# Performance work log

Measured on AMD Instinct MI355X. Metric: run time of the kernel, lower is better.

## Reference

```python
import jax, jax.numpy as jnp
import numpy as np

NPOINT = 1024   # npoint
K = 20          # num_samples[0]


def _fps(pts, npoint):
    """Iterative furthest point sampling. pts: [N,3] -> indices [npoint] (starts at idx 0)."""
    N = pts.shape[0]

    def step(carry, _):
        min_d, last = carry
        d = jnp.sum((pts - pts[last]) ** 2, axis=-1)          # [N] dist to last selected
        min_d = jnp.minimum(min_d, d)                          # running min-dist to selected set
        nxt = jnp.argmax(min_d).astype(jnp.int32)
        return (min_d, nxt), nxt

    init = (jnp.full((N,), 1e10, pts.dtype), jnp.int32(0))
    _, rest = jax.lax.scan(step, init, None, length=npoint - 1)
    return jnp.concatenate([jnp.zeros((1,), jnp.int32), rest])


def _pdist2(q, p):
    """Squared pairwise distances. q:[M,3], p:[N,3] -> [M,N], clamped to >=0 (matches pdist2squared)."""
    d = jnp.sum(q * q, -1)[:, None] + jnp.sum(p * p, -1)[None, :] - 2.0 * (q @ p.T)
    return jnp.maximum(d, 0.0)


def _knn(q, p, k):
    """k nearest neighbors of each q among p, dropping the closest (self), ascending order."""
    d = _pdist2(q, p)                       # [M,N]
    _, idx = jax.lax.top_k(-d, k + 1)       # ascending distance order
    return idx[:, 1:]                       # drop self, [M,k]


def setup_inputs() -> dict:
    key = jax.random.key(0)
    points = jax.random.normal(key, (4, 16384, 3), dtype=jnp.float32)
    return {"points": points}


def reference(points):
    B, N, _ = points.shape
    # --- FPS node sampling (Sample module) ---
    xyz_ind = jax.vmap(lambda p: _fps(p, NPOINT))(points)                  # [B, N1]
    xyz_query = jnp.take_along_axis(points, xyz_ind[:, :, None], axis=1)  # [B, N1, 3]

    # --- Gmid: neighbors of the N1 query points among all N points ---
    nbr_mid = jax.vmap(lambda q, p: _knn(q, p, K))(xyz_query, points)      # [B, N1, K]
    src_mid = jnp.take_along_axis(points, nbr_mid.reshape(B, -1, 1), axis=1).reshape(B, NPOINT, K, 3)
    d_mid = xyz_query[:, :, None, :] - src_mid                             # edata['d'] = pos[dst]-pos[src]

    # --- Gout: neighbors among the downsampled N1 points themselves ---
    nbr_out = jax.vmap(lambda q: _knn(q, q, K))(xyz_query)                 # [B, N1, K]
    src_out = jnp.take_along_axis(xyz_query, nbr_out.reshape(B, -1, 1), axis=1).reshape(B, NPOINT, K, 3)
    d_out = xyz_query[:, :, None, :] - src_out

    return xyz_ind, xyz_query, nbr_mid, d_mid, nbr_out, d_out
```

## Files before the change

### kernel.cpp

```cpp
#include <hip/hip_runtime.h>
#include <stdint.h>

#define BATCH   4
#define NPTS    16384
#define NPOINT  1024
#define KNN     20
#define KSEL    21

typedef unsigned long long u64;

#define FPS_SUBS 16
#define FPS_TPB  256
#define FPS_GT   (FPS_SUBS * FPS_TPB)
#define FPS_PPT  (NPTS / FPS_GT)

#define REPEAT4(M) M(0) M(1) M(2) M(3)

#define FPS_DECL(i) float px##i, py##i, pz##i, md##i;

#define FPS_INIT(i) { \
    int idx = (i) * FPS_GT + g; \
    px##i = P[idx * 3 + 0]; \
    py##i = P[idx * 3 + 1]; \
    pz##i = P[idx * 3 + 2]; \
    md##i = 1e10f; }

#define FPS_STEP(i) { \
    float dx = __fsub_rn(px##i, qx); \
    float dy = __fsub_rn(py##i, qy); \
    float dz = __fsub_rn(pz##i, qz); \
    float d  = __fadd_rn(__fadd_rn(__fmul_rn(dx, dx), __fmul_rn(dy, dy)), \
                         __fmul_rn(dz, dz)); \
    float m = fminf(md##i, d); \
    md##i = m; \
    bool g2 = (m > best); \
    best = g2 ? m : best; \
    bi   = g2 ? (i) : bi; }

__global__ __launch_bounds__(FPS_TPB)
void fps_kernel(const float* __restrict__ pts, float* __restrict__ out,
                int* __restrict__ ws_ind, float* __restrict__ ws_query,
                u64* __restrict__ slots) {
  const int blk = blockIdx.x;
  const int b   = blk >> 4;
  const int sub = blk & 15;
  const int t   = threadIdx.x;
  const int g   = sub * FPS_TPB + t;
  const float* P = pts + (size_t)b * NPTS * 3;
  float* out_ind = out;
  float* out_q   = out + BATCH * NPOINT;

  REPEAT4(FPS_DECL)
  REPEAT4(FPS_INIT)

  __shared__ float s_val[FPS_TPB / 64];
  __shared__ int   s_idx[FPS_TPB / 64];
  __shared__ int   s_widx;

  if (sub == 0 && t == 0) {
    out_ind[b * NPOINT] = 0.0f;
    ws_ind[b * NPOINT]  = 0;
    float ax = P[0], ay = P[1], az = P[2];
    size_t o0 = (size_t)(b * NPOINT) * 3;
    out_q[o0 + 0] = ax; out_q[o0 + 1] = ay; out_q[o0 + 2] = az;
    ws_query[o0 + 0] = ax; ws_query[o0 + 1] = ay; ws_query[o0 + 2] = az;
  }
  float qx = P[0], qy = P[1], qz = P[2];

  for (int it = 1; it < NPOINT; ++it) {
    float best = -1.0f;
    int bi = 0;
    REPEAT4(FPS_STEP)
    int bidx = bi * FPS_GT + g;

#pragma unroll
    for (int off = 32; off >= 1; off >>= 1) {
      float ov = __shfl_down(best, off);
      int   oi = __shfl_down(bidx, off);
      if (ov > best || (ov == best && oi < bidx)) { best = ov; bidx = oi; }
    }
    if ((t & 63) == 0) { s_val[t >> 6] = best; s_idx[t >> 6] = bidx; }
    __syncthreads();

    if (t < 64) {
      float bv = s_val[0];
      int   bx = s_idx[0];
#pragma unroll
      for (int w = 1; w < FPS_TPB / 64; ++w) {
        float v = s_val[w];
        int   x = s_idx[w];
        if (v > bv || (v == bv && x < bx)) { bv = v; bx = x; }
      }
      u64* row = slots + (size_t)it * (BATCH * FPS_SUBS) + b * FPS_SUBS;
      if (t == 0) {
        u64 pv = ((u64)__float_as_uint(bv) << 32) |
                 (unsigned)(bx | (it << 20));
        __hip_atomic_store(&row[sub], pv, __ATOMIC_RELAXED,
                           __HIP_MEMORY_SCOPE_AGENT);
      }
      int j = t & 15;
      u64 v;
      do {
        v = __hip_atomic_load(&row[j], __ATOMIC_RELAXED,
                              __HIP_MEMORY_SCOPE_AGENT);
      } while ((v >> 63) != 0 ||
               (((unsigned)(v >> 20)) & 0x3FFu) != (unsigned)it);
      float fv = __uint_as_float((unsigned)(v >> 32));
      int   fi = (int)((unsigned)v & 0xFFFFFu);
#pragma unroll
      for (int off = 8; off >= 1; off >>= 1) {
        float ofv = __shfl_down(fv, off);
        int   ofi = __shfl_down(fi, off);
        if (ofv > fv || (ofv == fv && ofi < fi)) { fv = ofv; fi = ofi; }
      }
      if (t == 0) s_widx = fi;
    }
    __syncthreads();
    const int widx = s_widx;

    qx = P[widx * 3 + 0];
    qy = P[widx * 3 + 1];
    qz = P[widx * 3 + 2];

    if (sub == 0 && t == 0) {
      out_ind[b * NPOINT + it] = (float)widx;
      ws_ind[b * NPOINT + it]  = widx;
      size_t o = (size_t)(b * NPOINT + it) * 3;
      out_q[o + 0] = qx; out_q[o + 1] = qy; out_q[o + 2] = qz;
      ws_query[o + 0] = qx; ws_query[o + 1] = qy; ws_query[o + 2] = qz;
    }
  }
}

#define KNN_WAVES 4

__global__ __launch_bounds__(256)
void knn_kernel(const float* __restrict__ cand_base,
                const float* __restrict__ query_base,
                int ncand,
                float* __restrict__ out_nbr,
                float* __restrict__ out_d) {
#pragma clang fp contract(off)
  const int wid_in_blk = threadIdx.x >> 6;
  const int w    = blockIdx.x * KNN_WAVES + wid_in_blk;
  const int lane = threadIdx.x & 63;
  const int b    = w / NPOINT;
  const int qi   = w % NPOINT;

  const float* C = cand_base + (size_t)b * ncand * 3;
  const float* Q = query_base + ((size_t)b * NPOINT + qi) * 3;
  const float qx = Q[0], qy = Q[1], qz = Q[2];
  const float qq = (qx * qx + qy * qy) + qz * qz;

  unsigned long long best[KSEL];
#pragma unroll
  for (int j = 0; j < KSEL; ++j) best[j] = 0xFFFFFFFFFFFFFFFFull;

  for (int j = lane; j < ncand; j += 64) {
    float px = C[j * 3 + 0], py = C[j * 3 + 1], pz = C[j * 3 + 2];
    float pp  = (px * px + py * py) + pz * pz;
    float dot = __builtin_fmaf(qz, pz, __builtin_fmaf(qy, py, qx * px));
    float d = (qq + pp) - 2.0f * dot;
    d = fmaxf(d, 0.0f);
    unsigned long long key =
        ((unsigned long long)__float_as_uint(d) << 32) | (unsigned int)j;
    if (key < best[KSEL - 1]) {
      unsigned long long c = key;
#pragma unroll
      for (int s = 0; s < KSEL; ++s) {
        unsigned long long o = best[s];
        bool l = c < o;
        unsigned long long nb = l ? c : o;
        c = l ? o : c;
        best[s] = nb;
      }
    }
  }

  __shared__ unsigned long long s_list[KNN_WAVES][64 * KSEL];
  unsigned long long* L = s_list[wid_in_blk];
#pragma unroll
  for (int j = 0; j < KSEL; ++j) L[lane * KSEL + j] = best[j];
  __syncthreads();

  int hp = 0;
  int myK = -1, myIdx = 0;
  for (int r = 0; r < KSEL; ++r) {
    unsigned long long v = L[lane * KSEL + hp];
    int src = lane;
#pragma unroll
    for (int off = 32; off >= 1; off >>= 1) {
      unsigned long long ov = __shfl_down(v, off);
      int os = __shfl_down(src, off);
      if (ov < v) { v = ov; src = os; }
    }
    v   = __shfl(v, 0);
    src = __shfl(src, 0);
    if (lane == src) hp++;
    if (r >= 1 && lane == r - 1) {
      myIdx = (int)(unsigned int)(v & 0xFFFFFFFFull);
      myK = r - 1;
    }
  }

  if (myK >= 0) {
    size_t o = (size_t)(b * NPOINT + qi) * KNN + myK;
    out_nbr[o] = (float)myIdx;
    float sx = C[myIdx * 3 + 0], sy = C[myIdx * 3 + 1], sz = C[myIdx * 3 + 2];
    out_d[o * 3 + 0] = qx - sx;
    out_d[o * 3 + 1] = qy - sy;
    out_d[o * 3 + 2] = qz - sz;
  }
}

extern "C" void kernel_launch(void* const* d_in, const int* in_sizes, int n_in,
                              void* d_out, int out_size, void* d_ws,
                              size_t ws_size, hipStream_t stream) {
  (void)in_sizes; (void)n_in; (void)out_size; (void)ws_size;
  const float* pts = (const float*)d_in[0];
  float* out = (float*)d_out;

  int*   ws_ind   = (int*)d_ws;
  float* ws_query = (float*)((char*)d_ws + (size_t)BATCH * NPOINT * sizeof(int));
  u64*   slots    = (u64*)((char*)d_ws + 64 * 1024);

  float* out_nbr_mid = out + (size_t)BATCH * NPOINT * 4;
  float* out_d_mid   = out_nbr_mid + (size_t)BATCH * NPOINT * KNN;
  float* out_nbr_out = out_d_mid + (size_t)BATCH * NPOINT * KNN * 3;
  float* out_d_out   = out_nbr_out + (size_t)BATCH * NPOINT * KNN;

  hipLaunchKernelGGL(fps_kernel, dim3(BATCH * FPS_SUBS), dim3(FPS_TPB), 0,
                     stream, pts, out, ws_ind, ws_query, slots);

  hipLaunchKernelGGL(knn_kernel, dim3(BATCH * NPOINT / KNN_WAVES), dim3(256),
                     0, stream, pts, ws_query, NPTS, out_nbr_mid, out_d_mid);

  hipLaunchKernelGGL(knn_kernel, dim3(BATCH * NPOINT / KNN_WAVES), dim3(256),
                     0, stream, ws_query, ws_query, NPOINT, out_nbr_out,
                     out_d_out);
}
```

Measured before the change: 2.786 ms.

## Fuse FPS and mid-KNN into one kernel, overlapping KNN with FPS progress

Merges the FPS kernel and the first KNN kernel into one launch. Extra blocks spin on the per-iteration FPS slot records to learn each selected index, then run their KNN query over the full point set while FPS is still iterating. The KNN merge step now keeps candidate lists in registers and walks the list head instead of staging them in shared memory. This hides most of the mid-KNN time behind the serial FPS loop. The risks are that spinning blocks compete with FPS blocks for compute units, and that the scheme relies on all FPS blocks being resident at once to avoid deadlock.

```diff
diff --git a/kernel.cpp b/kernel.cpp
--- a/kernel.cpp
+++ b/kernel.cpp
@@ -11,8 +11,10 @@
 
 #define FPS_SUBS 16
 #define FPS_TPB  256
+#define FPS_BLOCKS (BATCH * FPS_SUBS)
 #define FPS_GT   (FPS_SUBS * FPS_TPB)
 #define FPS_PPT  (NPTS / FPS_GT)
+#define KNN_BLOCKS (BATCH * NPOINT / 4)
 
 #define REPEAT4(M) M(0) M(1) M(2) M(3)
 
@@ -38,73 +40,122 @@
     bi   = g2 ? (i) : bi; }
 
 __global__ __launch_bounds__(FPS_TPB)
-void fps_kernel(const float* __restrict__ pts, float* __restrict__ out,
-                int* __restrict__ ws_ind, float* __restrict__ ws_query,
-                u64* __restrict__ slots) {
-  const int blk = blockIdx.x;
-  const int b   = blk >> 4;
-  const int sub = blk & 15;
-  const int t   = threadIdx.x;
-  const int g   = sub * FPS_TPB + t;
-  const float* P = pts + (size_t)b * NPTS * 3;
-  float* out_ind = out;
-  float* out_q   = out + BATCH * NPOINT;
-
-  REPEAT4(FPS_DECL)
-  REPEAT4(FPS_INIT)
-
+void fused_kernel(const float* __restrict__ pts, float* __restrict__ out,
+                  int* __restrict__ ws_ind, float* __restrict__ ws_query,
+                  u64* __restrict__ slots,
+                  float* __restrict__ out_nbr_mid,
+                  float* __restrict__ out_d_mid) {
   __shared__ float s_val[FPS_TPB / 64];
   __shared__ int   s_idx[FPS_TPB / 64];
   __shared__ int   s_widx;
 
-  if (sub == 0 && t == 0) {
-    out_ind[b * NPOINT] = 0.0f;
-    ws_ind[b * NPOINT]  = 0;
-    float ax = P[0], ay = P[1], az = P[2];
-    size_t o0 = (size_t)(b * NPOINT) * 3;
-    out_q[o0 + 0] = ax; out_q[o0 + 1] = ay; out_q[o0 + 2] = az;
-    ws_query[o0 + 0] = ax; ws_query[o0 + 1] = ay; ws_query[o0 + 2] = az;
-  }
-  float qx = P[0], qy = P[1], qz = P[2];
-
-  for (int it = 1; it < NPOINT; ++it) {
-    float best = -1.0f;
-    int bi = 0;
-    REPEAT4(FPS_STEP)
-    int bidx = bi * FPS_GT + g;
-
-#pragma unroll
-    for (int off = 32; off >= 1; off >>= 1) {
-      float ov = __shfl_down(best, off);
-      int   oi = __shfl_down(bidx, off);
-      if (ov > best || (ov == best && oi < bidx)) { best = ov; bidx = oi; }
-    }
-    if ((t & 63) == 0) { s_val[t >> 6] = best; s_idx[t >> 6] = bidx; }
-    __syncthreads();
-
-    if (t < 64) {
-      float bv = s_val[0];
-      int   bx = s_idx[0];
-#pragma unroll
-      for (int w = 1; w < FPS_TPB / 64; ++w) {
-        float v = s_val[w];
-        int   x = s_idx[w];
-        if (v > bv || (v == bv && x < bx)) { bv = v; bx = x; }
-      }
-      u64* row = slots + (size_t)it * (BATCH * FPS_SUBS) + b * FPS_SUBS;
-      if (t == 0) {
-        u64 pv = ((u64)__float_as_uint(bv) << 32) |
-                 (unsigned)(bx | (it << 20));
-        __hip_atomic_store(&row[sub], pv, __ATOMIC_RELAXED,
-                           __HIP_MEMORY_SCOPE_AGENT);
-      }
-      int j = t & 15;
+  if (blockIdx.x < FPS_BLOCKS) {
+    const int blk = blockIdx.x;
+    const int b   = blk >> 4;
+    const int sub = blk & 15;
+    const int t   = threadIdx.x;
+    const int g   = sub * FPS_TPB + t;
+    const float* P = pts + (size_t)b * NPTS * 3;
+    float* out_ind = out;
+    float* out_q   = out + BATCH * NPOINT;
+
+    REPEAT4(FPS_DECL)
+    REPEAT4(FPS_INIT)
+
+    if (sub == 0 && t == 0) {
+      out_ind[b * NPOINT] = 0.0f;
+      ws_ind[b * NPOINT]  = 0;
+      float ax = P[0], ay = P[1], az = P[2];
+      size_t o0 = (size_t)(b * NPOINT) * 3;
+      out_q[o0 + 0] = ax; out_q[o0 + 1] = ay; out_q[o0 + 2] = az;
+      ws_query[o0 + 0] = ax; ws_query[o0 + 1] = ay; ws_query[o0 + 2] = az;
+    }
+    float qx = P[0], qy = P[1], qz = P[2];
+
+    for (int it = 1; it < NPOINT; ++it) {
+      float best = -1.0f;
+      int bi = 0;
+      REPEAT4(FPS_STEP)
+      int bidx = bi * FPS_GT + g;
+
+#pragma unroll
+      for (int off = 32; off >= 1; off >>= 1) {
+        float ov = __shfl_down(best, off);
+        int   oi = __shfl_down(bidx, off);
+        if (ov > best || (ov == best && oi < bidx)) { best = ov; bidx = oi; }
+      }
+      if ((t & 63) == 0) { s_val[t >> 6] = best; s_idx[t >> 6] = bidx; }
+      __syncthreads();
+
+      if (t < 64) {
+        float bv = s_val[0];
+        int   bx = s_idx[0];
+#pragma unroll
+        for (int w = 1; w < FPS_TPB / 64; ++w) {
+          float v = s_val[w];
+          int   x = s_idx[w];
+          if (v > bv || (v == bv && x < bx)) { bv = v; bx = x; }
+        }
+        u64* row = slots + (size_t)it * (BATCH * FPS_SUBS) + b * FPS_SUBS;
+        if (t == 0) {
+          u64 pv = ((u64)__float_as_uint(bv) << 32) |
+                   (unsigned)(bx | (it << 20));
+          __hip_atomic_store(&row[sub], pv, __ATOMIC_RELAXED,
+                             __HIP_MEMORY_SCOPE_AGENT);
+        }
+        int j = t & 15;
+        u64 v;
+        do {
+          v = __hip_atomic_load(&row[j], __ATOMIC_RELAXED,
+                                __HIP_MEMORY_SCOPE_AGENT);
+        } while ((v >> 63) != 0 ||
+                 (((unsigned)(v >> 20)) & 0x3FFu) != (unsigned)it);
+        float fv = __uint_as_float((unsigned)(v >> 32));
+        int   fi = (int)((unsigned)v & 0xFFFFFu);
+#pragma unroll
+        for (int off = 8; off >= 1; off >>= 1) {
+          float ofv = __shfl_down(fv, off);
+          int   ofi = __shfl_down(fi, off);
+          if (ofv > fv || (ofv == fv && ofi < fi)) { fv = ofv; fi = ofi; }
+        }
+        if (t == 0) s_widx = fi;
+      }
+      __syncthreads();
+      const int widx = s_widx;
+
+      qx = P[widx * 3 + 0];
+      qy = P[widx * 3 + 1];
+      qz = P[widx * 3 + 2];
+
+      if (sub == 0 && t == 0) {
+        out_ind[b * NPOINT + it] = (float)widx;
+        ws_ind[b * NPOINT + it]  = widx;
+        size_t o = (size_t)(b * NPOINT + it) * 3;
+        out_q[o + 0] = qx; out_q[o + 1] = qy; out_q[o + 2] = qz;
+        ws_query[o + 0] = qx; ws_query[o + 1] = qy; ws_query[o + 2] = qz;
+      }
+    }
+  } else {
+#pragma clang fp contract(off)
+    const int wv   = (blockIdx.x - FPS_BLOCKS) * 4 + (threadIdx.x >> 6);
+    const int lane = threadIdx.x & 63;
+    const int b    = wv / NPOINT;
+    const int qi   = wv % NPOINT;
+    const float* C = pts + (size_t)b * NPTS * 3;
+
+    int widx = 0;
+    if (qi > 0) {
+      u64* row = slots + (size_t)qi * (BATCH * FPS_SUBS) + b * FPS_SUBS;
+      int j = lane & 15;
       u64 v;
-      do {
+      for (;;) {
         v = __hip_atomic_load(&row[j], __ATOMIC_RELAXED,
                               __HIP_MEMORY_SCOPE_AGENT);
-      } while ((v >> 63) != 0 ||
-               (((unsigned)(v >> 20)) & 0x3FFu) != (unsigned)it);
+        bool ok = ((v >> 63) == 0) &&
+                  ((((unsigned)(v >> 20)) & 0x3FFu) == (unsigned)qi);
+        if (__all(ok)) break;
+        __builtin_amdgcn_s_sleep(64);
+      }
       float fv = __uint_as_float((unsigned)(v >> 32));
       int   fi = (int)((unsigned)v & 0xFFFFFu);
 #pragma unroll
@@ -113,21 +164,73 @@
         int   ofi = __shfl_down(fi, off);
         if (ofv > fv || (ofv == fv && ofi < fi)) { fv = ofv; fi = ofi; }
       }
-      if (t == 0) s_widx = fi;
-    }
-    __syncthreads();
-    const int widx = s_widx;
-
-    qx = P[widx * 3 + 0];
-    qy = P[widx * 3 + 1];
-    qz = P[widx * 3 + 2];
-
-    if (sub == 0 && t == 0) {
-      out_ind[b * NPOINT + it] = (float)widx;
-      ws_ind[b * NPOINT + it]  = widx;
-      size_t o = (size_t)(b * NPOINT + it) * 3;
-      out_q[o + 0] = qx; out_q[o + 1] = qy; out_q[o + 2] = qz;
-      ws_query[o + 0] = qx; ws_query[o + 1] = qy; ws_query[o + 2] = qz;
+      widx = __shfl(fi, 0);
+    }
+
+    const float qx = C[widx * 3 + 0];
+    const float qy = C[widx * 3 + 1];
+    const float qz = C[widx * 3 + 2];
+    const float qq = (qx * qx + qy * qy) + qz * qz;
+
+    u64 best[KSEL];
+#pragma unroll
+    for (int j = 0; j < KSEL; ++j) best[j] = 0xFFFFFFFFFFFFFFFFull;
+
+    for (int j = lane; j < NPTS; j += 64) {
+      float px = C[j * 3 + 0], py = C[j * 3 + 1], pz = C[j * 3 + 2];
+      float pp  = (px * px + py * py) + pz * pz;
+      float dot = __builtin_fmaf(qz, pz, __builtin_fmaf(qy, py, qx * px));
+      float d = (qq + pp) - 2.0f * dot;
+      d = fmaxf(d, 0.0f);
+      u64 key = ((u64)__float_as_uint(d) << 32) | (unsigned)j;
+      if (key < best[KSEL - 1]) {
+        u64 c = key;
+#pragma unroll
+        for (int s = 0; s < KSEL; ++s) {
+          u64 o = best[s];
+          bool l = c < o;
+          u64 nb = l ? c : o;
+          c = l ? o : c;
+          best[s] = nb;
+        }
+      }
+    }
+
+    int hp = 1;
+    u64 head = best[0];
+    int myK = -1, myIdx = 0;
+#pragma unroll
+    for (int r = 0; r < KSEL; ++r) {
+      u64 v = head; int src = lane;
+#pragma unroll
+      for (int off = 32; off >= 1; off >>= 1) {
+        u64 ov = __shfl_down(v, off);
+        int os = __shfl_down(src, off);
+        if (ov < v) { v = ov; src = os; }
+      }
+      v   = __shfl(v, 0);
+      src = __shfl(src, 0);
+      if (r >= 1 && lane == r - 1) {
+        myIdx = (int)(unsigned)(v & 0xFFFFFFFFull);
+        myK = r - 1;
+      }
+      if (lane == src) {
+        u64 h = 0xFFFFFFFFFFFFFFFFull;
+#pragma unroll
+        for (int s = 1; s < KSEL; ++s) if (hp == s) h = best[s];
+        head = h;
+        hp++;
+      }
+    }
+
+    if (myK >= 0) {
+      size_t o = (size_t)(b * NPOINT + qi) * KNN + myK;
+      out_nbr_mid[o] = (float)myIdx;
+      float sx = C[myIdx * 3 + 0], sy = C[myIdx * 3 + 1],
+            sz = C[myIdx * 3 + 2];
+      out_d_mid[o * 3 + 0] = qx - sx;
+      out_d_mid[o * 3 + 1] = qy - sy;
+      out_d_mid[o * 3 + 2] = qz - sz;
     }
   }
 }
@@ -152,7 +255,7 @@
   const float qx = Q[0], qy = Q[1], qz = Q[2];
   const float qq = (qx * qx + qy * qy) + qz * qz;
 
-  unsigned long long best[KSEL];
+  u64 best[KSEL];
 #pragma unroll
   for (int j = 0; j < KSEL; ++j) best[j] = 0xFFFFFFFFFFFFFFFFull;
 
@@ -162,23 +265,22 @@
     float dot = __builtin_fmaf(qz, pz, __builtin_fmaf(qy, py, qx * px));
     float d = (qq + pp) - 2.0f * dot;
     d = fmaxf(d, 0.0f);
-    unsigned long long key =
-        ((unsigned long long)__float_as_uint(d) << 32) | (unsigned int)j;
+    u64 key = ((u64)__float_as_uint(d) << 32) | (unsigned)j;
     if (key < best[KSEL - 1]) {
-      unsigned long long c = key;
+      u64 c = key;
 #pragma unroll
       for (int s = 0; s < KSEL; ++s) {
-        unsigned long long o = best[s];
+        u64 o = best[s];
         bool l = c < o;
-        unsigned long long nb = l ? c : o;
+        u64 nb = l ? c : o;
         c = l ? o : c;
         best[s] = nb;
       }
     }
   }
 
-  __shared__ unsigned long long s_list[KNN_WAVES][64 * KSEL];
-  unsigned long long* L = s_list[wid_in_blk];
+  __shared__ u64 s_list[KNN_WAVES][64 * KSEL];
+  u64* L = s_list[wid_in_blk];
 #pragma unroll
   for (int j = 0; j < KSEL; ++j) L[lane * KSEL + j] = best[j];
   __syncthreads();
@@ -186,11 +288,11 @@
   int hp = 0;
   int myK = -1, myIdx = 0;
   for (int r = 0; r < KSEL; ++r) {
-    unsigned long long v = L[lane * KSEL + hp];
+    u64 v = L[lane * KSEL + hp];
     int src = lane;
 #pragma unroll
     for (int off = 32; off >= 1; off >>= 1) {
-      unsigned long long ov = __shfl_down(v, off);
+      u64 ov = __shfl_down(v, off);
       int os = __shfl_down(src, off);
       if (ov < v) { v = ov; src = os; }
     }
@@ -198,7 +300,7 @@
     src = __shfl(src, 0);
     if (lane == src) hp++;
     if (r >= 1 && lane == r - 1) {
-      myIdx = (int)(unsigned int)(v & 0xFFFFFFFFull);
+      myIdx = (int)(unsigned)(v & 0xFFFFFFFFull);
       myK = r - 1;
     }
   }
@@ -229,11 +331,10 @@
   float* out_nbr_out = out_d_mid + (size_t)BATCH * NPOINT * KNN * 3;
   float* out_d_out   = out_nbr_out + (size_t)BATCH * NPOINT * KNN;
 
-  hipLaunchKernelGGL(fps_kernel, dim3(BATCH * FPS_SUBS), dim3(FPS_TPB), 0,
-                     stream, pts, out, ws_ind, ws_query, slots);
-
-  hipLaunchKernelGGL(knn_kernel, dim3(BATCH * NPOINT / KNN_WAVES), dim3(256),
-                     0, stream, pts, ws_query, NPTS, out_nbr_mid, out_d_mid);
+  hipLaunchKernelGGL(fused_kernel, dim3(FPS_BLOCKS + KNN_BLOCKS),
+                     dim3(FPS_TPB), 0, stream,
+                     pts, out, ws_ind, ws_query, slots,
+                     out_nbr_mid, out_d_mid);
 
   hipLaunchKernelGGL(knn_kernel, dim3(BATCH * NPOINT / KNN_WAVES), dim3(256),
                      0, stream, ws_query, ws_query, NPOINT, out_nbr_out,
```

Result: no change. 2.737 ms (-1.7%).
